# Optimization experiments

Measured on AMD Instinct MI355X. Metric: run time of the kernel, lower is better.

Reference implementation:

```python
import jax, jax.numpy as jnp
import numpy as np

EPS = 1e-06

def elu_feature_map(x):
    return jax.nn.elu(x) + 1.0

def setup_inputs() -> dict:
    key = jax.random.key(0)
    kq, kk, kv, ks, kz = jax.random.split(key, 5)
    N, H, D, M = 2048, 16, 64, 64
    return {
        "query": jax.random.normal(kq, (N, H, D), dtype=jnp.float32),
        "key":   jax.random.normal(kk, (N, H, D), dtype=jnp.float32),
        "value": jax.random.normal(kv, (N, H, M), dtype=jnp.float32),
        "Si":    jax.random.normal(ks, (N, H, D, M), dtype=jnp.float32),
        "Zi":    jax.random.normal(kz, (N, H, D), dtype=jnp.float32),
    }

def reference(query, key, value, Si, Zi):
    Q = elu_feature_map(query)  # (N,H,D)
    K = elu_feature_map(key)    # (N,H,D)
    Zi_new = Zi + K                                        # (N,H,D)
    Si_new = Si + jnp.einsum('nhd,nhm->nhdm', K, value)    # (N,H,D,M)
    Z = 1.0 / (jnp.einsum('nhd,nhd->nh', Q, Zi_new) + EPS) # (N,H)
    V = jnp.einsum('nhd,nhdm,nh->nhm', Q, Si_new, Z)       # (N,H,M)
    return (V, Si_new, Zi_new)
```

## Files before the change

### kernel.cpp

```cpp
#include <hip/hip_runtime.h>
#include <math.h>

#define EPS 1e-6f

__global__ __launch_bounds__(256) void rla_kernel(
    const float* __restrict__ query,
    const float* __restrict__ key,
    const float* __restrict__ value,
    const float* __restrict__ Si,
    const float* __restrict__ Zi,
    float* __restrict__ Vout,
    float* __restrict__ Si_out,
    float* __restrict__ Zi_out)
{
    const int nh   = blockIdx.x;
    const int t    = threadIdx.x;
    const int col4 = t & 15;
    const int drow = t >> 4;

    __shared__ float Qs[64], Ks[64], Vs[64], Zin[64];
    __shared__ float Zsh;
    __shared__ float4 red[256];

    const size_t base64 = (size_t)nh * 64;

    if (t < 64) {
        float q = query[base64 + t];
        float k = key[base64 + t];
        float Qv = q > 0.f ? q + 1.f : expf(q);
        float Kv = k > 0.f ? k + 1.f : expf(k);
        Qs[t] = Qv;
        Ks[t] = Kv;
        Vs[t] = value[base64 + t];
        float zn = Zi[base64 + t] + Kv;
        Zin[t] = zn;
        Zi_out[base64 + t] = zn;
    }
    __syncthreads();

    if (t < 64) {
        float p = Qs[t] * Zin[t];
        #pragma unroll
        for (int off = 32; off >= 1; off >>= 1)
            p += __shfl_down(p, off);
        if (t == 0) Zsh = 1.f / (p + EPS);
    }
    __syncthreads();

    const float4* Si4 = (const float4*)(Si     + (size_t)nh * 4096);
    float4*       So4 = (float4*)      (Si_out + (size_t)nh * 4096);
    const float4  v4  = ((const float4*)Vs)[col4];

    float4 acc = make_float4(0.f, 0.f, 0.f, 0.f);
    #pragma unroll
    for (int kk = 0; kk < 4; ++kk) {
        const int f = t + 256 * kk;
        const int d = f >> 4;
        const float Kd = Ks[d];
        const float Qd = Qs[d];
        float4 si = Si4[f];
        float4 sn;
        sn.x = si.x + Kd * v4.x;
        sn.y = si.y + Kd * v4.y;
        sn.z = si.z + Kd * v4.z;
        sn.w = si.w + Kd * v4.w;
        So4[f] = sn;
        acc.x += Qd * sn.x;
        acc.y += Qd * sn.y;
        acc.z += Qd * sn.z;
        acc.w += Qd * sn.w;
    }

    red[t] = acc;
    __syncthreads();
    #pragma unroll
    for (int s = 8; s >= 1; s >>= 1) {
        if (drow < s) {
            float4 o = red[t + 16 * s];
            float4 m = red[t];
            m.x += o.x; m.y += o.y; m.z += o.z; m.w += o.w;
            red[t] = m;
        }
        __syncthreads();
    }
    if (drow == 0) {
        const float z = Zsh;
        float4 r = red[t];
        float4 outv;
        outv.x = r.x * z; outv.y = r.y * z; outv.z = r.z * z; outv.w = r.w * z;
        ((float4*)(Vout + base64))[col4] = outv;
    }
}

extern "C" void kernel_launch(void* const* d_in, const int* in_sizes, int n_in,
                              void* d_out, int out_size, void* d_ws, size_t ws_size,
                              hipStream_t stream) {
    const float* query = (const float*)d_in[0];
    const float* key   = (const float*)d_in[1];
    const float* value = (const float*)d_in[2];
    const float* Si    = (const float*)d_in[3];
    const float* Zi    = (const float*)d_in[4];

    const int NH = in_sizes[0] / 64;
    float* out    = (float*)d_out;
    float* Vout   = out;
    float* Si_out = out + (size_t)NH * 64;
    float* Zi_out = Si_out + (size_t)NH * 4096;

    rla_kernel<<<NH, 256, 0, stream>>>(query, key, value, Si, Zi,
                                       Vout, Si_out, Zi_out);
}
```

Baseline: 201.5 us.

## Map one wavefront per head and replace shared-memory reductions with shuffles

Each 64-lane wavefront now handles one (n,h) pair, with four per block. Cross-lane shuffles broadcast K, Q and V and perform both reductions, which removes shared memory and all block barriers. The Si read and Si_out write now use nontemporal load and store builtins, and fast __expf is used. Each lane now streams 16 float4s instead of 4, which adds per-thread work and shuffle overhead. The grid assumes NH is divisible by 4.

```diff
diff --git a/kernel.cpp b/kernel.cpp
--- a/kernel.cpp
+++ b/kernel.cpp
@@ -2,6 +2,8 @@
 #include <math.h>
 
 #define EPS 1e-6f
+
+typedef float floatx4 __attribute__((ext_vector_type(4)));
 
 __global__ __launch_bounds__(256) void rla_kernel(
     const float* __restrict__ query,
@@ -13,82 +15,61 @@
     float* __restrict__ Si_out,
     float* __restrict__ Zi_out)
 {
-    const int nh   = blockIdx.x;
-    const int t    = threadIdx.x;
-    const int col4 = t & 15;
-    const int drow = t >> 4;
-
-    __shared__ float Qs[64], Ks[64], Vs[64], Zin[64];
-    __shared__ float Zsh;
-    __shared__ float4 red[256];
+    const int wid  = threadIdx.x >> 6;
+    const int lane = threadIdx.x & 63;
+    const int nh   = blockIdx.x * 4 + wid;
 
     const size_t base64 = (size_t)nh * 64;
 
-    if (t < 64) {
-        float q = query[base64 + t];
-        float k = key[base64 + t];
-        float Qv = q > 0.f ? q + 1.f : expf(q);
-        float Kv = k > 0.f ? k + 1.f : expf(k);
-        Qs[t] = Qv;
-        Ks[t] = Kv;
-        Vs[t] = value[base64 + t];
-        float zn = Zi[base64 + t] + Kv;
-        Zin[t] = zn;
-        Zi_out[base64 + t] = zn;
-    }
-    __syncthreads();
+    float q  = query[base64 + lane];
+    float k  = key[base64 + lane];
+    float Qv = q > 0.f ? q + 1.f : __expf(q);
+    float Kv = k > 0.f ? k + 1.f : __expf(k);
+    float vv = value[base64 + lane];
+    float zn = Zi[base64 + lane] + Kv;
+    Zi_out[base64 + lane] = zn;
 
-    if (t < 64) {
-        float p = Qs[t] * Zin[t];
-        #pragma unroll
-        for (int off = 32; off >= 1; off >>= 1)
-            p += __shfl_down(p, off);
-        if (t == 0) Zsh = 1.f / (p + EPS);
-    }
-    __syncthreads();
+    float p = Qv * zn;
+    #pragma unroll
+    for (int off = 32; off >= 1; off >>= 1)
+        p += __shfl_xor(p, off);
+    const float Zinv = 1.f / (p + EPS);
 
-    const float4* Si4 = (const float4*)(Si     + (size_t)nh * 4096);
-    float4*       So4 = (float4*)      (Si_out + (size_t)nh * 4096);
-    const float4  v4  = ((const float4*)Vs)[col4];
+    const int col4 = lane & 15;
+    const int dgrp = lane >> 4;
 
-    float4 acc = make_float4(0.f, 0.f, 0.f, 0.f);
+    floatx4 v4;
+    v4.x = __shfl(vv, 4 * col4 + 0);
+    v4.y = __shfl(vv, 4 * col4 + 1);
+    v4.z = __shfl(vv, 4 * col4 + 2);
+    v4.w = __shfl(vv, 4 * col4 + 3);
+
+    const floatx4* Si4 = (const floatx4*)(Si     + (size_t)nh * 4096);
+    floatx4*       So4 = (floatx4*)      (Si_out + (size_t)nh * 4096);
+
+    floatx4 acc = (floatx4)0.f;
     #pragma unroll
-    for (int kk = 0; kk < 4; ++kk) {
-        const int f = t + 256 * kk;
-        const int d = f >> 4;
-        const float Kd = Ks[d];
-        const float Qd = Qs[d];
-        float4 si = Si4[f];
-        float4 sn;
-        sn.x = si.x + Kd * v4.x;
-        sn.y = si.y + Kd * v4.y;
-        sn.z = si.z + Kd * v4.z;
-        sn.w = si.w + Kd * v4.w;
-        So4[f] = sn;
-        acc.x += Qd * sn.x;
-        acc.y += Qd * sn.y;
-        acc.z += Qd * sn.z;
-        acc.w += Qd * sn.w;
+    for (int kk = 0; kk < 16; ++kk) {
+        const int f = lane + (kk << 6);
+        const int d = dgrp + (kk << 2);
+        const float Kd = __shfl(Kv, d);
+        const float Qd = __shfl(Qv, d);
+        floatx4 si = __builtin_nontemporal_load(&Si4[f]);
+        floatx4 sn = si + Kd * v4;
+        __builtin_nontemporal_store(sn, &So4[f]);
+        acc += Qd * sn;
     }
 
-    red[t] = acc;
-    __syncthreads();
     #pragma unroll
-    for (int s = 8; s >= 1; s >>= 1) {
-        if (drow < s) {
-            float4 o = red[t + 16 * s];
-            float4 m = red[t];
-            m.x += o.x; m.y += o.y; m.z += o.z; m.w += o.w;
-            red[t] = m;
-        }
-        __syncthreads();
+    for (int off = 32; off >= 16; off >>= 1) {
+        acc.x += __shfl_xor(acc.x, off);
+        acc.y += __shfl_xor(acc.y, off);
+        acc.z += __shfl_xor(acc.z, off);
+        acc.w += __shfl_xor(acc.w, off);
     }
-    if (drow == 0) {
-        const float z = Zsh;
-        float4 r = red[t];
-        float4 outv;
-        outv.x = r.x * z; outv.y = r.y * z; outv.z = r.z * z; outv.w = r.w * z;
-        ((float4*)(Vout + base64))[col4] = outv;
+    if (lane < 16) {
+        floatx4 outv = acc * Zinv;
+        ((floatx4*)(Vout + base64))[lane] = outv;
     }
 }
 
@@ -107,6 +88,6 @@
     float* Si_out = out + (size_t)NH * 64;
     float* Zi_out = Si_out + (size_t)NH * 4096;
 
-    rla_kernel<<<NH, 256, 0, stream>>>(query, key, value, Si, Zi,
-                                       Vout, Si_out, Zi_out);
+    rla_kernel<<<NH / 4, 256, 0, stream>>>(query, key, value, Si, Zi,
+                                           Vout, Si_out, Zi_out);
 }
```

Result: faster. 186.1 us (-7.6%).
